# Kernel optimization log

Hardware: AMD Instinct MI355X
Metric: run time of the kernel (lower is better)

Reference implementation:

```python
import jax, jax.numpy as jnp
import numpy as np

N_NODES = 100000
N_EDGES = 1600000
N_GRAPHS = 512
IN_DIM, HID, OUT_DIM = 11, 64, 16
SOFTPLUS_BIAS = float(np.log(np.expm1(1.0)))  # biased_softplus_1.0 from NormalParamExtractor
SCALE_LB = 1e-4


def _glorot(key, shape):
    lim = float(np.sqrt(6.0 / (shape[0] + shape[1])))
    return jax.random.uniform(key, shape, jnp.float32, -lim, lim)


def setup_inputs() -> dict:
    key = jax.random.key(0)
    ks = jax.random.split(key, 12)
    x = jax.random.normal(ks[0], (N_NODES, IN_DIM), jnp.float32)
    edge_index = jax.random.randint(ks[1], (2, N_EDGES), 0, N_NODES, jnp.int64)
    batch = jnp.sort(jax.random.randint(ks[2], (N_NODES,), 0, N_GRAPHS, jnp.int64))
    params = {
        'W0': _glorot(ks[3], (IN_DIM, HID)), 'b0': jnp.zeros((HID,), jnp.float32),
        'Wrel1': _glorot(ks[4], (HID, HID)), 'brel1': jnp.zeros((HID,), jnp.float32),
        'Wroot1': _glorot(ks[5], (HID, HID)),
        'Wrel2': _glorot(ks[6], (HID, HID)), 'brel2': jnp.zeros((HID,), jnp.float32),
        'Wroot2': _glorot(ks[7], (HID, HID)),
        'W3': _glorot(ks[8], (HID, OUT_DIM)), 'b3': jnp.zeros((OUT_DIM,), jnp.float32),
    }
    return dict(x=x, edge_index=edge_index, batch=batch, **params)


def _graph_conv(x, src, dst, Wrel, brel, Wroot):
    # PyG GraphConv (aggr='add'): out = lin_rel(sum_{j in N(i)} x_j) + lin_root(x_i)
    agg = jax.ops.segment_sum(x[src], dst, num_segments=N_NODES)
    return agg @ Wrel + brel + x @ Wroot


def reference(x, edge_index, batch, W0, b0, Wrel1, brel1, Wroot1, Wrel2, brel2, Wroot2, W3, b3):
    src, dst = edge_index[0], edge_index[1]
    h = x @ W0 + b0                                   # [N, 64]
    h = jnp.tanh(_graph_conv(h, src, dst, Wrel1, brel1, Wroot1))
    h = jnp.tanh(_graph_conv(h, src, dst, Wrel2, brel2, Wroot2))
    h = jnp.tanh(h @ W3 + b3)                         # [N, 16]
    sums = jax.ops.segment_sum(h, batch, num_segments=N_GRAPHS)
    cnts = jax.ops.segment_sum(jnp.ones((h.shape[0],), h.dtype), batch, num_segments=N_GRAPHS)
    pooled = sums / jnp.maximum(cnts, 1.0)[:, None]   # [B, 16] global_mean_pool
    loc, scale_raw = jnp.split(pooled, 2, axis=-1)    # NormalParamExtractor
    scale = jnp.maximum(jax.nn.softplus(scale_raw + SOFTPLUS_BIAS), SCALE_LB)
    return loc, scale
```

## Files before the change

### kernel.cpp

```cpp
#include <hip/hip_runtime.h>
#include <hip/hip_bf16.h>
#include <math.h>


#define CAP 64
#define FILL_PARTS 8
#define FILL_BPP 1024
typedef __hip_bfloat16 bf16;
typedef __attribute__((ext_vector_type(8))) short bf16x8;
typedef __attribute__((ext_vector_type(4))) float f32x4;

__global__ __launch_bounds__(256) void k_in(const float* __restrict__ x,
    const float* __restrict__ W0, const float* __restrict__ b0,
    bf16* __restrict__ h, int N) {
  __shared__ float w[11 * 64];
  __shared__ float xl[4][12];
  int tid = threadIdx.x;
  for (int i = tid; i < 11 * 64; i += 256) w[i] = W0[i];
  int row0 = blockIdx.x * 4;
  if (tid < 44) {
    int r = tid / 11, k = tid % 11;
    int g = row0 + r;
    xl[r][k] = (g < N) ? x[(size_t)g * 11 + k] : 0.f;
  }
  __syncthreads();
  int c = tid & 63, r = tid >> 6;
  int g = row0 + r;
  float acc = b0[c];
#pragma unroll
  for (int k = 0; k < 11; ++k) acc += xl[r][k] * w[k * 64 + c];
  if (g < N) h[(size_t)g * 64 + c] = __float2bfloat16(acc);
}

__global__ __launch_bounds__(256) void k_fill(const int* __restrict__ ei,
    int* __restrict__ cnt, int* __restrict__ csr, int E, int N) {
  int p  = blockIdx.x & 7;
  int sb = blockIdx.x >> 3;
  int nb = gridDim.x >> 3;
  int part = (N + 7) >> 3;
  int lo = p * part, hi = min(N, lo + part);
  const int* src = ei;
  const int* dst = ei + E;
  int E4 = E >> 2;
  const int4* d4 = (const int4*)dst;
  for (int i = sb * 256 + threadIdx.x; i < E4; i += nb * 256) {
    int4 dv = d4[i];
#pragma unroll
    for (int k = 0; k < 4; ++k) {
      int d = (&dv.x)[k];
      if (d >= lo && d < hi) {
        int s = src[i * 4 + k];
        int pos = atomicAdd(&cnt[d], 1);
        if (pos < CAP) csr[(size_t)d * CAP + pos] = s;
      }
    }
  }
  if (sb == 0 && threadIdx.x < (E & 3)) {
    int e = (E4 << 2) + threadIdx.x;
    int d = dst[e];
    if (d >= lo && d < hi) {
      int s = src[e];
      int pos = atomicAdd(&cnt[d], 1);
      if (pos < CAP) csr[(size_t)d * CAP + pos] = s;
    }
  }
}

__global__ __launch_bounds__(256) void k_gather(const bf16* __restrict__ h,
    const int* __restrict__ csr, const int* __restrict__ cnt,
    bf16* __restrict__ agg, int N) {
  int wid = __builtin_amdgcn_readfirstlane(threadIdx.x >> 6);
  int node = blockIdx.x * 4 + wid;
  if (node >= N) return;
  int c = threadIdx.x & 63;
  int deg = min(cnt[node], CAP);
  int myidx = csr[(size_t)node * CAP + c];
  float a0 = 0.f, a1 = 0.f, a2 = 0.f, a3 = 0.f;
  int j = 0;
  for (; j + 4 <= deg; j += 4) {
    int s0 = __shfl(myidx, j + 0);
    int s1 = __shfl(myidx, j + 1);
    int s2 = __shfl(myidx, j + 2);
    int s3 = __shfl(myidx, j + 3);
    a0 += __bfloat162float(h[(size_t)s0 * 64 + c]);
    a1 += __bfloat162float(h[(size_t)s1 * 64 + c]);
    a2 += __bfloat162float(h[(size_t)s2 * 64 + c]);
    a3 += __bfloat162float(h[(size_t)s3 * 64 + c]);
  }
  for (; j < deg; ++j)
    a0 += __bfloat162float(h[(size_t)__shfl(myidx, j) * 64 + c]);
  agg[(size_t)node * 64 + c] = __float2bfloat16((a0 + a1) + (a2 + a3));
}

__global__ __launch_bounds__(256) void k_convm(const bf16* A, const bf16* H,
    const float* __restrict__ Wrel, const float* __restrict__ brel,
    const float* __restrict__ Wroot, bf16* out, int N) {
  __shared__ float wlds[2][64 * 64];
  int tid = threadIdx.x;
  for (int i = tid * 4; i < 64 * 64; i += 1024) {
    *(float4*)(&wlds[0][i]) = *(const float4*)(Wrel + i);
    *(float4*)(&wlds[1][i]) = *(const float4*)(Wroot + i);
  }
  __syncthreads();
  int lane = tid & 63;
  int wv = __builtin_amdgcn_readfirstlane(tid >> 6);
  int lr = lane & 15;
  int lk = lane >> 4;

  bf16x8 wr[4][2], wo[4][2];
#pragma unroll
  for (int cb = 0; cb < 4; ++cb) {
#pragma unroll
    for (int ks = 0; ks < 2; ++ks) {
      bf16* pr = (bf16*)&wr[cb][ks];
      bf16* po = (bf16*)&wo[cb][ks];
#pragma unroll
      for (int i = 0; i < 8; ++i) {
        int k = lk * 8 + i + ks * 32;
        int col = lr + cb * 16;
        pr[i] = __float2bfloat16(wlds[0][k * 64 + col]);
        po[i] = __float2bfloat16(wlds[1][k * 64 + col]);
      }
    }
  }
  float bias[4];
#pragma unroll
  for (int cb = 0; cb < 4; ++cb) bias[cb] = brel[lr + cb * 16];

  int rb = blockIdx.x * 64 + wv * 16;
  if (rb >= N) return;
  int arow = min(rb + lr, N - 1);
  const bf16x8* Ap = (const bf16x8*)(A + (size_t)arow * 64 + lk * 8);
  const bf16x8* Hp = (const bf16x8*)(H + (size_t)arow * 64 + lk * 8);
  bf16x8 a0 = Ap[0], a1 = Ap[4];
  bf16x8 h0 = Hp[0], h1 = Hp[4];

  f32x4 acc[4];
#pragma unroll
  for (int cb = 0; cb < 4; ++cb) {
    f32x4 c0 = {bias[cb], bias[cb], bias[cb], bias[cb]};
    c0 = __builtin_amdgcn_mfma_f32_16x16x32_bf16(a0, wr[cb][0], c0, 0, 0, 0);
    c0 = __builtin_amdgcn_mfma_f32_16x16x32_bf16(a1, wr[cb][1], c0, 0, 0, 0);
    c0 = __builtin_amdgcn_mfma_f32_16x16x32_bf16(h0, wo[cb][0], c0, 0, 0, 0);
    c0 = __builtin_amdgcn_mfma_f32_16x16x32_bf16(h1, wo[cb][1], c0, 0, 0, 0);
    acc[cb] = c0;
  }
#pragma unroll
  for (int cb = 0; cb < 4; ++cb) {
#pragma unroll
    for (int r = 0; r < 4; ++r) {
      int row = rb + lk * 4 + r;
      if (row < N)
        out[(size_t)row * 64 + lr + cb * 16] = __float2bfloat16(tanhf(acc[cb][r]));
    }
  }
}

__global__ __launch_bounds__(256) void k_h3(const bf16* __restrict__ h2,
    const float* __restrict__ W3, const float* __restrict__ b3,
    float* __restrict__ h3, int N) {
  __shared__ float w[64 * 16];
  int tid = threadIdx.x;
  for (int i = tid; i < 64 * 16; i += 256) w[i] = W3[i];
  __syncthreads();
  int c = tid & 15, rg = tid >> 4;
  int row0 = blockIdx.x * 64;
#pragma unroll
  for (int i = 0; i < 4; ++i) {
    int row = row0 + rg + i * 16;
    int rowc = min(row, N - 1);
    float acc = b3[c];
    for (int k8 = 0; k8 < 64; k8 += 8) {
      bf16 hv[8];
      *(uint4*)hv = *(const uint4*)(h2 + (size_t)rowc * 64 + k8);
#pragma unroll
      for (int kk = 0; kk < 8; ++kk)
        acc += __bfloat162float(hv[kk]) * w[(k8 + kk) * 16 + c];
    }
    if (row < N) h3[(size_t)row * 16 + c] = tanhf(acc);
  }
}

__global__ __launch_bounds__(256) void k_pool(const float* __restrict__ h3,
    const int* __restrict__ batch, float* __restrict__ out, int N, int B) {
  __shared__ int srange[2];
  __shared__ float red[256];
  int b = blockIdx.x;
  int tid = threadIdx.x;
  if (tid < 2) {
    int target = b + tid;
    int lo = 0, hi = N;
    while (lo < hi) {
      int mid = (lo + hi) >> 1;
      if (batch[mid] < target) lo = mid + 1; else hi = mid;
    }
    srange[tid] = lo;
  }
  __syncthreads();
  int s = srange[0], e = srange[1];
  int f = tid & 15, g = tid >> 4;
  float acc = 0.f;
  for (int n = s + g; n < e; n += 16) acc += h3[(size_t)n * 16 + f];
  red[tid] = acc;
  __syncthreads();
  for (int stride = 128; stride >= 16; stride >>= 1) {
    if (tid < stride) red[tid] += red[tid + stride];
    __syncthreads();
  }
  if (tid < 16) {
    float cnt = (float)(e - s);
    float pooled = red[tid] / fmaxf(cnt, 1.0f);
    if (tid < 8) {
      out[(size_t)b * 8 + tid] = pooled;
    } else {
      float xx = pooled + 0.54132485461292f;
      float sp = (xx > 20.f) ? xx : log1pf(expf(xx));
      out[(size_t)B * 8 + (size_t)b * 8 + (tid - 8)] = fmaxf(sp, 1e-4f);
    }
  }
}

extern "C" void kernel_launch(void* const* d_in, const int* in_sizes, int n_in,
                              void* d_out, int out_size, void* d_ws, size_t ws_size,
                              hipStream_t stream) {
  const float* x      = (const float*)d_in[0];
  const int*   ei     = (const int*)d_in[1];
  const int*   batch  = (const int*)d_in[2];
  const float* W0     = (const float*)d_in[3];
  const float* b0     = (const float*)d_in[4];
  const float* Wrel1  = (const float*)d_in[5];
  const float* brel1  = (const float*)d_in[6];
  const float* Wroot1 = (const float*)d_in[7];
  const float* Wrel2  = (const float*)d_in[8];
  const float* brel2  = (const float*)d_in[9];
  const float* Wroot2 = (const float*)d_in[10];
  const float* W3     = (const float*)d_in[11];
  const float* b3     = (const float*)d_in[12];
  float* out = (float*)d_out;

  int N = in_sizes[0] / 11;
  int E = in_sizes[1] / 2;
  int B = out_size / 16;

  bf16*  hb   = (bf16*)d_ws;
  bf16*  aggb = hb + (size_t)N * 64;
  float* h3b  = (float*)(aggb + (size_t)N * 64);
  int*   cnt  = (int*)(h3b + (size_t)N * 16);
  int*   csr  = cnt + N;

  int nst = (N + 63) / 64;

  hipMemsetAsync(cnt, 0, (size_t)N * sizeof(int), stream);
  k_in<<<(N + 3) / 4, 256, 0, stream>>>(x, W0, b0, hb, N);
  k_fill<<<FILL_PARTS * FILL_BPP, 256, 0, stream>>>(ei, cnt, csr, E, N);

  k_gather<<<(N + 3) / 4, 256, 0, stream>>>(hb, csr, cnt, aggb, N);
  k_convm<<<nst, 256, 0, stream>>>(aggb, hb, Wrel1, brel1, Wroot1, hb, N);

  k_gather<<<(N + 3) / 4, 256, 0, stream>>>(hb, csr, cnt, aggb, N);
  k_convm<<<nst, 256, 0, stream>>>(aggb, hb, Wrel2, brel2, Wroot2, aggb, N);

  k_h3<<<(N + 63) / 64, 256, 0, stream>>>(aggb, W3, b3, h3b, N);
  k_pool<<<B, 256, 0, stream>>>(h3b, batch, out, N, B);
}
```

Measured before the change: 312.4 us.

## Fuse neighbor gather with GraphConv MFMA and fold output projection into second layer

Merges the per-node CSR gather and the dense GraphConv MFMA into one kernel. Aggregated rows stay in LDS tiles instead of round-tripping through a global agg buffer, and weights are staged transposed in LDS as bf16. The second layer also applies the W3 projection and tanh via MFMA, removing the separate h3 kernel. This cuts launches and global traffic, but each wave now gathers 16 nodes serially with 64 nodes per block, which may lower memory-level parallelism for the latency-bound gather.

```diff
diff --git a/kernel.cpp b/kernel.cpp
--- a/kernel.cpp
+++ b/kernel.cpp
@@ -66,118 +66,103 @@
   }
 }
 
-__global__ __launch_bounds__(256) void k_gather(const bf16* __restrict__ h,
-    const int* __restrict__ csr, const int* __restrict__ cnt,
-    bf16* __restrict__ agg, int N) {
-  int wid = __builtin_amdgcn_readfirstlane(threadIdx.x >> 6);
-  int node = blockIdx.x * 4 + wid;
-  if (node >= N) return;
-  int c = threadIdx.x & 63;
-  int deg = min(cnt[node], CAP);
-  int myidx = csr[(size_t)node * CAP + c];
-  float a0 = 0.f, a1 = 0.f, a2 = 0.f, a3 = 0.f;
-  int j = 0;
-  for (; j + 4 <= deg; j += 4) {
-    int s0 = __shfl(myidx, j + 0);
-    int s1 = __shfl(myidx, j + 1);
-    int s2 = __shfl(myidx, j + 2);
-    int s3 = __shfl(myidx, j + 3);
-    a0 += __bfloat162float(h[(size_t)s0 * 64 + c]);
-    a1 += __bfloat162float(h[(size_t)s1 * 64 + c]);
-    a2 += __bfloat162float(h[(size_t)s2 * 64 + c]);
-    a3 += __bfloat162float(h[(size_t)s3 * 64 + c]);
-  }
-  for (; j < deg; ++j)
-    a0 += __bfloat162float(h[(size_t)__shfl(myidx, j) * 64 + c]);
-  agg[(size_t)node * 64 + c] = __float2bfloat16((a0 + a1) + (a2 + a3));
-}
-
-__global__ __launch_bounds__(256) void k_convm(const bf16* A, const bf16* H,
-    const float* __restrict__ Wrel, const float* __restrict__ brel,
-    const float* __restrict__ Wroot, bf16* out, int N) {
-  __shared__ float wlds[2][64 * 64];
+template <int DO_H3>
+__global__ __launch_bounds__(256) void k_gconv(
+    const bf16* __restrict__ hin, const int* __restrict__ csr,
+    const int* __restrict__ cnt, const float* __restrict__ Wrel,
+    const float* __restrict__ brel, const float* __restrict__ Wroot,
+    const float* __restrict__ W3, const float* __restrict__ b3,
+    bf16* __restrict__ hout, float* __restrict__ h3out, int N) {
+  __shared__ bf16 wT[2][64][72];
+  __shared__ bf16 tile[4][16][72];
   int tid = threadIdx.x;
-  for (int i = tid * 4; i < 64 * 64; i += 1024) {
-    *(float4*)(&wlds[0][i]) = *(const float4*)(Wrel + i);
-    *(float4*)(&wlds[1][i]) = *(const float4*)(Wroot + i);
-  }
-  __syncthreads();
+  for (int j = tid; j < 4096; j += 256) {
+    int k = j >> 6, col = j & 63;
+    wT[0][col][k] = __float2bfloat16(Wrel[j]);
+    wT[1][col][k] = __float2bfloat16(Wroot[j]);
+  }
   int lane = tid & 63;
   int wv = __builtin_amdgcn_readfirstlane(tid >> 6);
-  int lr = lane & 15;
-  int lk = lane >> 4;
-
-  bf16x8 wr[4][2], wo[4][2];
+  int rb = blockIdx.x * 64;
+  for (int t = 0; t < 16; ++t) {
+    int n = rb + wv * 16 + t;
+    float a0 = 0.f, a1 = 0.f, a2 = 0.f, a3 = 0.f;
+    if (n < N) {
+      int deg = min(cnt[n], CAP);
+      int myidx = csr[(size_t)n * CAP + lane];
+      int j = 0;
+      for (; j + 4 <= deg; j += 4) {
+        int s0 = __shfl(myidx, j + 0);
+        int s1 = __shfl(myidx, j + 1);
+        int s2 = __shfl(myidx, j + 2);
+        int s3 = __shfl(myidx, j + 3);
+        a0 += __bfloat162float(hin[(size_t)s0 * 64 + lane]);
+        a1 += __bfloat162float(hin[(size_t)s1 * 64 + lane]);
+        a2 += __bfloat162float(hin[(size_t)s2 * 64 + lane]);
+        a3 += __bfloat162float(hin[(size_t)s3 * 64 + lane]);
+      }
+      for (; j < deg; ++j)
+        a0 += __bfloat162float(hin[(size_t)__shfl(myidx, j) * 64 + lane]);
+    }
+    tile[wv][t][lane] = __float2bfloat16((a0 + a1) + (a2 + a3));
+  }
+  __syncthreads();
+  int lr = lane & 15, lk = lane >> 4;
+  bf16x8 a0 = *(const bf16x8*)&tile[wv][lr][lk * 8];
+  bf16x8 a1 = *(const bf16x8*)&tile[wv][lr][lk * 8 + 32];
+  int hrow = min(rb + wv * 16 + lr, N - 1);
+  const bf16x8* Hp = (const bf16x8*)(hin + (size_t)hrow * 64 + lk * 8);
+  bf16x8 h0 = Hp[0], h1 = Hp[4];
+  f32x4 acc[4];
 #pragma unroll
   for (int cb = 0; cb < 4; ++cb) {
-#pragma unroll
-    for (int ks = 0; ks < 2; ++ks) {
-      bf16* pr = (bf16*)&wr[cb][ks];
-      bf16* po = (bf16*)&wo[cb][ks];
-#pragma unroll
-      for (int i = 0; i < 8; ++i) {
-        int k = lk * 8 + i + ks * 32;
-        int col = lr + cb * 16;
-        pr[i] = __float2bfloat16(wlds[0][k * 64 + col]);
-        po[i] = __float2bfloat16(wlds[1][k * 64 + col]);
+    bf16x8 br0 = *(const bf16x8*)&wT[0][cb * 16 + lr][lk * 8];
+    bf16x8 br1 = *(const bf16x8*)&wT[0][cb * 16 + lr][lk * 8 + 32];
+    bf16x8 bo0 = *(const bf16x8*)&wT[1][cb * 16 + lr][lk * 8];
+    bf16x8 bo1 = *(const bf16x8*)&wT[1][cb * 16 + lr][lk * 8 + 32];
+    float bb = brel[cb * 16 + lr];
+    f32x4 c0 = {bb, bb, bb, bb};
+    c0 = __builtin_amdgcn_mfma_f32_16x16x32_bf16(a0, br0, c0, 0, 0, 0);
+    c0 = __builtin_amdgcn_mfma_f32_16x16x32_bf16(a1, br1, c0, 0, 0, 0);
+    c0 = __builtin_amdgcn_mfma_f32_16x16x32_bf16(h0, bo0, c0, 0, 0, 0);
+    c0 = __builtin_amdgcn_mfma_f32_16x16x32_bf16(h1, bo1, c0, 0, 0, 0);
+    acc[cb] = c0;
+  }
+  if (!DO_H3) {
+#pragma unroll
+    for (int cb = 0; cb < 4; ++cb)
+#pragma unroll
+      for (int r = 0; r < 4; ++r) {
+        int row = rb + wv * 16 + lk * 4 + r;
+        if (row < N)
+          hout[(size_t)row * 64 + cb * 16 + lr] = __float2bfloat16(tanhf(acc[cb][r]));
       }
-    }
-  }
-  float bias[4];
-#pragma unroll
-  for (int cb = 0; cb < 4; ++cb) bias[cb] = brel[lr + cb * 16];
-
-  int rb = blockIdx.x * 64 + wv * 16;
-  if (rb >= N) return;
-  int arow = min(rb + lr, N - 1);
-  const bf16x8* Ap = (const bf16x8*)(A + (size_t)arow * 64 + lk * 8);
-  const bf16x8* Hp = (const bf16x8*)(H + (size_t)arow * 64 + lk * 8);
-  bf16x8 a0 = Ap[0], a1 = Ap[4];
-  bf16x8 h0 = Hp[0], h1 = Hp[4];
-
-  f32x4 acc[4];
-#pragma unroll
-  for (int cb = 0; cb < 4; ++cb) {
-    f32x4 c0 = {bias[cb], bias[cb], bias[cb], bias[cb]};
-    c0 = __builtin_amdgcn_mfma_f32_16x16x32_bf16(a0, wr[cb][0], c0, 0, 0, 0);
-    c0 = __builtin_amdgcn_mfma_f32_16x16x32_bf16(a1, wr[cb][1], c0, 0, 0, 0);
-    c0 = __builtin_amdgcn_mfma_f32_16x16x32_bf16(h0, wo[cb][0], c0, 0, 0, 0);
-    c0 = __builtin_amdgcn_mfma_f32_16x16x32_bf16(h1, wo[cb][1], c0, 0, 0, 0);
-    acc[cb] = c0;
-  }
-#pragma unroll
-  for (int cb = 0; cb < 4; ++cb) {
+  } else {
+#pragma unroll
+    for (int cb = 0; cb < 4; ++cb)
+#pragma unroll
+      for (int r = 0; r < 4; ++r)
+        tile[wv][lk * 4 + r][cb * 16 + lr] = __float2bfloat16(tanhf(acc[cb][r]));
+    __syncthreads();
+    bf16x8 p0 = *(const bf16x8*)&tile[wv][lr][lk * 8];
+    bf16x8 p1 = *(const bf16x8*)&tile[wv][lr][lk * 8 + 32];
+    bf16x8 q0, q1;
+    bf16* q0p = (bf16*)&q0;
+    bf16* q1p = (bf16*)&q1;
+#pragma unroll
+    for (int i = 0; i < 8; ++i) {
+      q0p[i] = __float2bfloat16(W3[(lk * 8 + i) * 16 + lr]);
+      q1p[i] = __float2bfloat16(W3[(lk * 8 + i + 32) * 16 + lr]);
+    }
+    float b3v = b3[lr];
+    f32x4 c3 = {b3v, b3v, b3v, b3v};
+    c3 = __builtin_amdgcn_mfma_f32_16x16x32_bf16(p0, q0, c3, 0, 0, 0);
+    c3 = __builtin_amdgcn_mfma_f32_16x16x32_bf16(p1, q1, c3, 0, 0, 0);
 #pragma unroll
     for (int r = 0; r < 4; ++r) {
-      int row = rb + lk * 4 + r;
-      if (row < N)
-        out[(size_t)row * 64 + lr + cb * 16] = __float2bfloat16(tanhf(acc[cb][r]));
-    }
-  }
-}
-
-__global__ __launch_bounds__(256) void k_h3(const bf16* __restrict__ h2,
-    const float* __restrict__ W3, const float* __restrict__ b3,
-    float* __restrict__ h3, int N) {
-  __shared__ float w[64 * 16];
-  int tid = threadIdx.x;
-  for (int i = tid; i < 64 * 16; i += 256) w[i] = W3[i];
-  __syncthreads();
-  int c = tid & 15, rg = tid >> 4;
-  int row0 = blockIdx.x * 64;
-#pragma unroll
-  for (int i = 0; i < 4; ++i) {
-    int row = row0 + rg + i * 16;
-    int rowc = min(row, N - 1);
-    float acc = b3[c];
-    for (int k8 = 0; k8 < 64; k8 += 8) {
-      bf16 hv[8];
-      *(uint4*)hv = *(const uint4*)(h2 + (size_t)rowc * 64 + k8);
-#pragma unroll
-      for (int kk = 0; kk < 8; ++kk)
-        acc += __bfloat162float(hv[kk]) * w[(k8 + kk) * 16 + c];
-    }
-    if (row < N) h3[(size_t)row * 16 + c] = tanhf(acc);
+      int row = rb + wv * 16 + lk * 4 + r;
+      if (row < N) h3out[(size_t)row * 16 + lr] = tanhf(c3[r]);
+    }
   }
 }
 
@@ -243,8 +228,8 @@
   int B = out_size / 16;
 
   bf16*  hb   = (bf16*)d_ws;
-  bf16*  aggb = hb + (size_t)N * 64;
-  float* h3b  = (float*)(aggb + (size_t)N * 64);
+  bf16*  h1b  = hb + (size_t)N * 64;
+  float* h3b  = (float*)(h1b + (size_t)N * 64);
   int*   cnt  = (int*)(h3b + (size_t)N * 16);
   int*   csr  = cnt + N;
 
@@ -254,12 +239,10 @@
   k_in<<<(N + 3) / 4, 256, 0, stream>>>(x, W0, b0, hb, N);
   k_fill<<<FILL_PARTS * FILL_BPP, 256, 0, stream>>>(ei, cnt, csr, E, N);
 
-  k_gather<<<(N + 3) / 4, 256, 0, stream>>>(hb, csr, cnt, aggb, N);
-  k_convm<<<nst, 256, 0, stream>>>(aggb, hb, Wrel1, brel1, Wroot1, hb, N);
-
-  k_gather<<<(N + 3) / 4, 256, 0, stream>>>(hb, csr, cnt, aggb, N);
-  k_convm<<<nst, 256, 0, stream>>>(aggb, hb, Wrel2, brel2, Wroot2, aggb, N);
-
-  k_h3<<<(N + 63) / 64, 256, 0, stream>>>(aggb, W3, b3, h3b, N);
+  k_gconv<0><<<nst, 256, 0, stream>>>(hb, csr, cnt, Wrel1, brel1, Wroot1,
+                                      nullptr, nullptr, h1b, nullptr, N);
+  k_gconv<1><<<nst, 256, 0, stream>>>(h1b, csr, cnt, Wrel2, brel2, Wroot2,
+                                      W3, b3, nullptr, h3b, N);
+
   k_pool<<<B, 256, 0, stream>>>(h3b, batch, out, N, B);
 }
```

Result: slower. 358.7 us (+14.8%).

## Vectorize neighbor gather and fuse output projection into second conv kernel

Applied to the files above, without the earlier changes.

The gather kernel now has each lane load four bf16 features at once, 16 lanes covering a row, with four neighbor rows in flight per iteration and a cross-lane shuffle reduction at the end. This replaces one scalar 2-byte load per lane per neighbor. The second GraphConv kernel gains a template mode that stages its tanh output in LDS and applies the 64x16 W3 projection with MFMA. This removes the separate k_h3 launch and the write and re-read of h2. The cost is extra shuffle reductions in the gather, and an LDS tile plus uncached W3 global reads in every block.

```diff
diff --git a/kernel.cpp b/kernel.cpp
--- a/kernel.cpp
+++ b/kernel.cpp
@@ -9,6 +9,9 @@
 typedef __hip_bfloat16 bf16;
 typedef __attribute__((ext_vector_type(8))) short bf16x8;
 typedef __attribute__((ext_vector_type(4))) float f32x4;
+
+__device__ inline float bflo(unsigned u) { return __uint_as_float(u << 16); }
+__device__ inline float bfhi(unsigned u) { return __uint_as_float(u & 0xFFFF0000u); }
 
 __global__ __launch_bounds__(256) void k_in(const float* __restrict__ x,
     const float* __restrict__ W0, const float* __restrict__ b0,
@@ -66,40 +69,56 @@
   }
 }
 
-__global__ __launch_bounds__(256) void k_gather(const bf16* __restrict__ h,
+__global__ __launch_bounds__(256) void k_gather(const bf16* __restrict__ hin,
     const int* __restrict__ csr, const int* __restrict__ cnt,
     bf16* __restrict__ agg, int N) {
-  int wid = __builtin_amdgcn_readfirstlane(threadIdx.x >> 6);
-  int node = blockIdx.x * 4 + wid;
+  int wv = __builtin_amdgcn_readfirstlane(threadIdx.x >> 6);
+  int node = blockIdx.x * 4 + wv;
   if (node >= N) return;
-  int c = threadIdx.x & 63;
+  int lane = threadIdx.x & 63;
   int deg = min(cnt[node], CAP);
-  int myidx = csr[(size_t)node * CAP + c];
-  float a0 = 0.f, a1 = 0.f, a2 = 0.f, a3 = 0.f;
-  int j = 0;
-  for (; j + 4 <= deg; j += 4) {
-    int s0 = __shfl(myidx, j + 0);
-    int s1 = __shfl(myidx, j + 1);
-    int s2 = __shfl(myidx, j + 2);
-    int s3 = __shfl(myidx, j + 3);
-    a0 += __bfloat162float(h[(size_t)s0 * 64 + c]);
-    a1 += __bfloat162float(h[(size_t)s1 * 64 + c]);
-    a2 += __bfloat162float(h[(size_t)s2 * 64 + c]);
-    a3 += __bfloat162float(h[(size_t)s3 * 64 + c]);
-  }
-  for (; j < deg; ++j)
-    a0 += __bfloat162float(h[(size_t)__shfl(myidx, j) * 64 + c]);
-  agg[(size_t)node * 64 + c] = __float2bfloat16((a0 + a1) + (a2 + a3));
-}
-
+  int myidx = csr[(size_t)node * CAP + lane];
+  int fg = lane & 15, rg = lane >> 4;
+  float s0 = 0.f, s1 = 0.f, s2 = 0.f, s3 = 0.f;
+  for (int j = 0; j < deg; j += 8) {
+    int l0 = j + rg, l1 = j + 4 + rg;
+    int i0 = __shfl(myidx, min(l0, deg - 1));
+    int i1 = __shfl(myidx, min(l1, deg - 1));
+    uint2 u0 = *(const uint2*)(hin + (size_t)i0 * 64 + fg * 4);
+    uint2 u1 = *(const uint2*)(hin + (size_t)i1 * 64 + fg * 4);
+    if (l0 < deg) {
+      s0 += bflo(u0.x); s1 += bfhi(u0.x);
+      s2 += bflo(u0.y); s3 += bfhi(u0.y);
+    }
+    if (l1 < deg) {
+      s0 += bflo(u1.x); s1 += bfhi(u1.x);
+      s2 += bflo(u1.y); s3 += bfhi(u1.y);
+    }
+  }
+  s0 += __shfl_xor(s0, 16); s0 += __shfl_xor(s0, 32);
+  s1 += __shfl_xor(s1, 16); s1 += __shfl_xor(s1, 32);
+  s2 += __shfl_xor(s2, 16); s2 += __shfl_xor(s2, 32);
+  s3 += __shfl_xor(s3, 16); s3 += __shfl_xor(s3, 32);
+  if (rg == 0) {
+    bf16 o[4] = {__float2bfloat16(s0), __float2bfloat16(s1),
+                 __float2bfloat16(s2), __float2bfloat16(s3)};
+    *(uint2*)(agg + (size_t)node * 64 + fg * 4) = *(uint2*)o;
+  }
+}
+
+template <int DO_H3>
 __global__ __launch_bounds__(256) void k_convm(const bf16* A, const bf16* H,
     const float* __restrict__ Wrel, const float* __restrict__ brel,
-    const float* __restrict__ Wroot, bf16* out, int N) {
-  __shared__ float wlds[2][64 * 64];
+    const float* __restrict__ Wroot, const float* __restrict__ W3,
+    const float* __restrict__ b3, bf16* hout, float* __restrict__ h3out,
+    int N) {
+  extern __shared__ char smem[];
+  float* wlds = (float*)smem;
+  bf16* tile = (bf16*)(smem + 32768);
   int tid = threadIdx.x;
   for (int i = tid * 4; i < 64 * 64; i += 1024) {
-    *(float4*)(&wlds[0][i]) = *(const float4*)(Wrel + i);
-    *(float4*)(&wlds[1][i]) = *(const float4*)(Wroot + i);
+    *(float4*)(wlds + i) = *(const float4*)(Wrel + i);
+    *(float4*)(wlds + 4096 + i) = *(const float4*)(Wroot + i);
   }
   __syncthreads();
   int lane = tid & 63;
@@ -118,15 +137,11 @@
       for (int i = 0; i < 8; ++i) {
         int k = lk * 8 + i + ks * 32;
         int col = lr + cb * 16;
-        pr[i] = __float2bfloat16(wlds[0][k * 64 + col]);
-        po[i] = __float2bfloat16(wlds[1][k * 64 + col]);
+        pr[i] = __float2bfloat16(wlds[k * 64 + col]);
+        po[i] = __float2bfloat16(wlds[4096 + k * 64 + col]);
       }
     }
   }
-  float bias[4];
-#pragma unroll
-  for (int cb = 0; cb < 4; ++cb) bias[cb] = brel[lr + cb * 16];
-
   int rb = blockIdx.x * 64 + wv * 16;
   if (rb >= N) return;
   int arow = min(rb + lr, N - 1);
@@ -138,46 +153,49 @@
   f32x4 acc[4];
 #pragma unroll
   for (int cb = 0; cb < 4; ++cb) {
-    f32x4 c0 = {bias[cb], bias[cb], bias[cb], bias[cb]};
+    float bb = brel[cb * 16 + lr];
+    f32x4 c0 = {bb, bb, bb, bb};
     c0 = __builtin_amdgcn_mfma_f32_16x16x32_bf16(a0, wr[cb][0], c0, 0, 0, 0);
     c0 = __builtin_amdgcn_mfma_f32_16x16x32_bf16(a1, wr[cb][1], c0, 0, 0, 0);
     c0 = __builtin_amdgcn_mfma_f32_16x16x32_bf16(h0, wo[cb][0], c0, 0, 0, 0);
     c0 = __builtin_amdgcn_mfma_f32_16x16x32_bf16(h1, wo[cb][1], c0, 0, 0, 0);
     acc[cb] = c0;
   }
-#pragma unroll
-  for (int cb = 0; cb < 4; ++cb) {
+  if (!DO_H3) {
+#pragma unroll
+    for (int cb = 0; cb < 4; ++cb)
+#pragma unroll
+      for (int r = 0; r < 4; ++r) {
+        int row = rb + lk * 4 + r;
+        if (row < N)
+          hout[(size_t)row * 64 + cb * 16 + lr] = __float2bfloat16(tanhf(acc[cb][r]));
+      }
+  } else {
+    bf16* mytile = tile + wv * 16 * 72;
+#pragma unroll
+    for (int cb = 0; cb < 4; ++cb)
+#pragma unroll
+      for (int r = 0; r < 4; ++r)
+        mytile[(lk * 4 + r) * 72 + cb * 16 + lr] = __float2bfloat16(tanhf(acc[cb][r]));
+    bf16x8 p0 = *(const bf16x8*)&mytile[lr * 72 + lk * 8];
+    bf16x8 p1 = *(const bf16x8*)&mytile[lr * 72 + lk * 8 + 32];
+    bf16x8 q0, q1;
+    bf16* q0p = (bf16*)&q0;
+    bf16* q1p = (bf16*)&q1;
+#pragma unroll
+    for (int i = 0; i < 8; ++i) {
+      q0p[i] = __float2bfloat16(W3[(lk * 8 + i) * 16 + lr]);
+      q1p[i] = __float2bfloat16(W3[(lk * 8 + i + 32) * 16 + lr]);
+    }
+    float b3v = b3[lr];
+    f32x4 c3 = {b3v, b3v, b3v, b3v};
+    c3 = __builtin_amdgcn_mfma_f32_16x16x32_bf16(p0, q0, c3, 0, 0, 0);
+    c3 = __builtin_amdgcn_mfma_f32_16x16x32_bf16(p1, q1, c3, 0, 0, 0);
 #pragma unroll
     for (int r = 0; r < 4; ++r) {
       int row = rb + lk * 4 + r;
-      if (row < N)
-        out[(size_t)row * 64 + lr + cb * 16] = __float2bfloat16(tanhf(acc[cb][r]));
-    }
-  }
-}
-
-__global__ __launch_bounds__(256) void k_h3(const bf16* __restrict__ h2,
-    const float* __restrict__ W3, const float* __restrict__ b3,
-    float* __restrict__ h3, int N) {
-  __shared__ float w[64 * 16];
-  int tid = threadIdx.x;
-  for (int i = tid; i < 64 * 16; i += 256) w[i] = W3[i];
-  __syncthreads();
-  int c = tid & 15, rg = tid >> 4;
-  int row0 = blockIdx.x * 64;
-#pragma unroll
-  for (int i = 0; i < 4; ++i) {
-    int row = row0 + rg + i * 16;
-    int rowc = min(row, N - 1);
-    float acc = b3[c];
-    for (int k8 = 0; k8 < 64; k8 += 8) {
-      bf16 hv[8];
-      *(uint4*)hv = *(const uint4*)(h2 + (size_t)rowc * 64 + k8);
-#pragma unroll
-      for (int kk = 0; kk < 8; ++kk)
-        acc += __bfloat162float(hv[kk]) * w[(k8 + kk) * 16 + c];
-    }
-    if (row < N) h3[(size_t)row * 16 + c] = tanhf(acc);
+      if (row < N) h3out[(size_t)row * 16 + lr] = tanhf(c3[r]);
+    }
   }
 }
 
@@ -255,11 +273,11 @@
   k_fill<<<FILL_PARTS * FILL_BPP, 256, 0, stream>>>(ei, cnt, csr, E, N);
 
   k_gather<<<(N + 3) / 4, 256, 0, stream>>>(hb, csr, cnt, aggb, N);
-  k_convm<<<nst, 256, 0, stream>>>(aggb, hb, Wrel1, brel1, Wroot1, hb, N);
-
+  k_convm<0><<<nst, 256, 32768, stream>>>(aggb, hb, Wrel1, brel1, Wroot1,
+                                          nullptr, nullptr, hb, nullptr, N);
   k_gather<<<(N + 3) / 4, 256, 0, stream>>>(hb, csr, cnt, aggb, N);
-  k_convm<<<nst, 256, 0, stream>>>(aggb, hb, Wrel2, brel2, Wroot2, aggb, N);
-
-  k_h3<<<(N + 63) / 64, 256, 0, stream>>>(aggb, W3, b3, h3b, N);
+  k_convm<1><<<nst, 256, 32768 + 4 * 16 * 72 * 2, stream>>>(
+      aggb, hb, Wrel2, brel2, Wroot2, W3, b3, nullptr, h3b, N);
+
   k_pool<<<B, 256, 0, stream>>>(h3b, batch, out, N, B);
 }
```

Result: faster. 290.5 us (-7.0%).
